# Performance work log

Hardware: AMD Instinct MI355X
Metric: run time of the kernel (lower is better)

The kernel has to match this reference:

```python
import jax, jax.numpy as jnp
import numpy as np

B, C, H, W = 8, 64, 256, 256   # input images
FH, FW = 64, 64                # low-res feature map
S = 256                        # superpixels per image (num[i] == S)


def setup_inputs() -> dict:
    key = jax.random.key(0)
    k1, k2, k3 = jax.random.split(key, 3)
    inp = jax.random.normal(k1, (B, C, H, W), dtype=jnp.float32)
    feat = jax.random.normal(k2, (B, C, FH, FW), dtype=jnp.float32)
    sp = jax.random.randint(k3, (B, 1, H, W), 0, S).astype(jnp.int64)
    num = jnp.full((B,), S, dtype=jnp.int64)
    return {"input": inp, "feature": feat, "sp": sp, "num": num}


def bilinear_align_corners(x, out_h, out_w):
    # F.interpolate(x, size, mode='bilinear', align_corners=True)
    _, _, in_h, in_w = x.shape
    ys = jnp.linspace(0.0, in_h - 1.0, out_h)
    xs = jnp.linspace(0.0, in_w - 1.0, out_w)
    y0 = jnp.floor(ys).astype(jnp.int32)
    x0 = jnp.floor(xs).astype(jnp.int32)
    y1 = jnp.minimum(y0 + 1, in_h - 1)
    x1 = jnp.minimum(x0 + 1, in_w - 1)
    wy = (ys - y0.astype(ys.dtype)).reshape(1, 1, out_h, 1)
    wx = (xs - x0.astype(xs.dtype)).reshape(1, 1, 1, out_w)
    rows = x[:, :, y0, :] * (1.0 - wy) + x[:, :, y1, :] * wy   # [B,C,out_h,in_w]
    return rows[:, :, :, x0] * (1.0 - wx) + rows[:, :, :, x1] * wx


def segment_scalar_means(x, sp, num):
    # torch: mean_values[i][j] = mean(x[i][sp[i]==j]) over channels AND pixels
    b = x.shape[0]
    px = x.mean(axis=1).reshape(b, -1)           # channel-mean per pixel [B, HW]
    ids = sp.reshape(b, -1)                      # [B, HW]
    seg_sum = jax.vmap(lambda v, i: jax.ops.segment_sum(v, i, num_segments=S))(px, ids)
    seg_cnt = jax.vmap(lambda i: jax.ops.segment_sum(jnp.ones(i.shape, jnp.float32), i, num_segments=S))(ids)
    m = jnp.where(seg_cnt > 0, seg_sum / jnp.maximum(seg_cnt, 1.0), 0.0)  # nan_to_num(0)
    valid = jnp.arange(S)[None, :] < num[:, None]                          # j < num[i]
    return jnp.where(valid, m, 0.0)              # [B, S]


def similarity_matrix(m):
    # mean_values broadcast to [B,S,C] => 1 - ||diff||/sqrt(C) == 1 - |m_j - m_k|
    return 1.0 - jnp.abs(m[:, :, None] - m[:, None, :])   # [B, S, S]


def reference(input, feature, sp, num):
    feat = bilinear_align_corners(feature, input.shape[-1], input.shape[-1])
    mat1 = similarity_matrix(segment_scalar_means(input, sp, num))
    mat2 = similarity_matrix(segment_scalar_means(feat, sp, num))
    return jnp.mean(jnp.abs(mat1 - mat2))   # nn.L1Loss()
```

## Files before the change

### kernel.cpp

```cpp
#include <hip/hip_runtime.h>

#define NB 8
#define NC 64
#define NH 256
#define NW 256
#define HW (NH*NW)
#define NFH 64
#define NFW 64
#define FHW (NFH*NFW)
#define NS 256
#define PPB 1024
#define NPB (HW/PPB)
#define NG 4
#define CPG (NC/NG)
#define NA (NB*NPB*NG)
#define NBB (NB*NPB)

__global__ __launch_bounds__(256) void fmean_k(const float* __restrict__ feature,
                                               float* __restrict__ fmean) {
  int idx = blockIdx.x * 256 + threadIdx.x;
  int b = idx >> 10;
  int q = idx & 1023;
  const float4* src = reinterpret_cast<const float4*>(feature + (size_t)b * NC * FHW) + q;
  float4 a = make_float4(0.f, 0.f, 0.f, 0.f);
  #pragma unroll 16
  for (int c = 0; c < NC; ++c) {
    float4 v = src[(size_t)c * (FHW / 4)];
    a.x += v.x; a.y += v.y; a.z += v.z; a.w += v.w;
  }
  const float s = 1.0f / NC;
  a.x *= s; a.y *= s; a.z *= s; a.w *= s;
  reinterpret_cast<float4*>(fmean)[idx] = a;
}

__global__ __launch_bounds__(256) void
main_k(const float* __restrict__ input,
       const int* __restrict__ sp,
       const float* __restrict__ fmean,
       float* __restrict__ part1,
       float* __restrict__ part2,
       float* __restrict__ partc) {
  __shared__ float s_f[FHW];
  __shared__ float s_bins[NS];
  __shared__ unsigned s_cnt[NS];

  const int bid = blockIdx.x;
  const int tid = threadIdx.x;

  if (bid < NA) {
    const int g  = bid & (NG - 1);
    const int pb = (bid >> 2) & (NPB - 1);
    const int b  = bid >> 8;

    s_bins[tid] = 0.f;
    __syncthreads();

    const int p0 = pb * PPB + tid * 4;
    const float* ib = input + ((size_t)(b * NC + g * CPG)) * HW + p0;
    float4 acc = make_float4(0.f, 0.f, 0.f, 0.f);
    #pragma unroll
    for (int c = 0; c < CPG; ++c) {
      float4 v = *reinterpret_cast<const float4*>(ib + (size_t)c * HW);
      acc.x += v.x; acc.y += v.y; acc.z += v.z; acc.w += v.w;
    }
    const float s = 1.0f / NC;
    int4 idv = *reinterpret_cast<const int4*>(sp + (size_t)b * HW + p0);
    atomicAdd(&s_bins[idv.x], acc.x * s);
    atomicAdd(&s_bins[idv.y], acc.y * s);
    atomicAdd(&s_bins[idv.z], acc.z * s);
    atomicAdd(&s_bins[idv.w], acc.w * s);
    __syncthreads();

    part1[(size_t)bid * NS + tid] = s_bins[tid];
  } else {
    const int r  = bid - NA;
    const int b  = r >> 6;
    const int pb = r & (NPB - 1);

    const float4* fsrc = reinterpret_cast<const float4*>(fmean + (size_t)b * FHW);
    #pragma unroll
    for (int i = 0; i < 4; ++i)
      reinterpret_cast<float4*>(s_f)[tid + 256 * i] = fsrc[tid + 256 * i];
    s_bins[tid] = 0.f;
    s_cnt[tid] = 0u;
    __syncthreads();

    const int p0 = pb * PPB + tid * 4;
    int4 idv = *reinterpret_cast<const int4*>(sp + (size_t)b * HW + p0);
    int ids[4] = {idv.x, idv.y, idv.z, idv.w};

    const int h = p0 >> 8;
    const float yd = (float)h * (63.0f / 255.0f);
    const int y0 = (int)yd;
    const float wy = yd - (float)y0;
    const int y1 = min(y0 + 1, NFH - 1);
    const float* row0 = s_f + y0 * NFW;
    const float* row1 = s_f + y1 * NFW;

    #pragma unroll
    for (int i = 0; i < 4; ++i) {
      const int w = (p0 & 255) + i;
      const float xd = (float)w * (63.0f / 255.0f);
      const int x0 = (int)xd;
      const float wx = xd - (float)x0;
      const int x1 = min(x0 + 1, NFW - 1);
      float top = row0[x0] * (1.f - wx) + row0[x1] * wx;
      float bot = row1[x0] * (1.f - wx) + row1[x1] * wx;
      float fv = top * (1.f - wy) + bot * wy;
      atomicAdd(&s_bins[ids[i]], fv);
      atomicAdd(&s_cnt[ids[i]], 1u);
    }
    __syncthreads();

    part2[(size_t)r * NS + tid] = s_bins[tid];
    partc[(size_t)r * NS + tid] = (float)s_cnt[tid];
  }
}

__global__ __launch_bounds__(256) void
finalize_k(const float* __restrict__ part1,
           const float* __restrict__ part2,
           const float* __restrict__ partc,
           const int* __restrict__ num,
           float* __restrict__ partial) {
  __shared__ float m1[NS];
  __shared__ float m2[NS];
  __shared__ float red[256];
  const int b = blockIdx.x;
  const int j = threadIdx.x;

  float s1 = 0.f;
  const float* p1 = part1 + (size_t)b * 256 * NS + j;
  #pragma unroll 8
  for (int t = 0; t < 256; ++t) s1 += p1[(size_t)t * NS];

  float s2 = 0.f, c = 0.f;
  const float* p2 = part2 + (size_t)b * 64 * NS + j;
  const float* pc = partc + (size_t)b * 64 * NS + j;
  #pragma unroll 8
  for (int t = 0; t < 64; ++t) { s2 += p2[(size_t)t * NS]; c += pc[(size_t)t * NS]; }

  const int nb = num[b];
  float v1 = 0.f, v2 = 0.f;
  if (j < nb && c > 0.f) {
    float invc = 1.0f / c;
    v1 = s1 * invc;
    v2 = s2 * invc;
  }
  m1[j] = v1; m2[j] = v2;
  __syncthreads();

  float accum = 0.f;
  #pragma unroll 8
  for (int k = 0; k < NS; ++k) {
    accum += fabsf(fabsf(v1 - m1[k]) - fabsf(v2 - m2[k]));
  }
  red[j] = accum;
  __syncthreads();
  for (int s = 128; s > 0; s >>= 1) {
    if (j < s) red[j] += red[j + s];
    __syncthreads();
  }
  if (j == 0) partial[b] = red[0];
}

__global__ void final_k(const float* __restrict__ partial, float* __restrict__ out) {
  if (threadIdx.x == 0 && blockIdx.x == 0) {
    float s = 0.f;
    for (int b = 0; b < NB; ++b) s += partial[b];
    out[0] = s / (float)((long long)NB * NS * NS);
  }
}

extern "C" void kernel_launch(void* const* d_in, const int* in_sizes, int n_in,
                              void* d_out, int out_size, void* d_ws, size_t ws_size,
                              hipStream_t stream) {
  const float* input   = (const float*)d_in[0];
  const float* feature = (const float*)d_in[1];
  const int*   sp      = (const int*)d_in[2];
  const int*   num     = (const int*)d_in[3];
  float* out = (float*)d_out;

  float* ws      = (float*)d_ws;
  float* part1   = ws;
  float* part2   = ws + (size_t)NA * NS;
  float* partc   = part2 + (size_t)NBB * NS;
  float* fmean   = partc + (size_t)NBB * NS;
  float* partial = fmean + NB * FHW;

  fmean_k<<<32, 256, 0, stream>>>(feature, fmean);
  main_k<<<NA + NBB, 256, 0, stream>>>(input, sp, fmean, part1, part2, partc);
  finalize_k<<<NB, 256, 0, stream>>>(part1, part2, partc, num, partial);
  final_k<<<1, 64, 0, stream>>>(partial, out);
}
```

Before: 56.66 us.

## Widen feature-mean kernel, merge feature blocks into main, fold final reduction

The channel-mean kernel for the feature map now runs on 256 blocks, with each block splitting channels across warps and reducing through shared memory, so it is no longer limited to 32 blocks. The separate feature-binning blocks are merged into the g==0 input blocks, which removes 512 extra blocks but makes those blocks heavier. The last finalize block now does the cross-batch sum using an atomic counter, which drops the final_k launch. The counter is reset inside main_k, and correctness depends on that reset being ordered before finalize runs.

Measured after the change: 63.02 us. 1.11x slower.

```diff
diff --git a/kernel.cpp b/kernel.cpp
--- a/kernel.cpp
+++ b/kernel.cpp
@@ -13,24 +13,38 @@
 #define NPB (HW/PPB)
 #define NG 4
 #define CPG (NC/NG)
-#define NA (NB*NPB*NG)
-#define NBB (NB*NPB)
+#define NMAIN (NB*NPB*NG)
+#define NRB (NB*NPB)
 
 __global__ __launch_bounds__(256) void fmean_k(const float* __restrict__ feature,
                                                float* __restrict__ fmean) {
-  int idx = blockIdx.x * 256 + threadIdx.x;
-  int b = idx >> 10;
-  int q = idx & 1023;
-  const float4* src = reinterpret_cast<const float4*>(feature + (size_t)b * NC * FHW) + q;
+  __shared__ float4 s_p[8][32];
+  const int b     = blockIdx.x >> 5;
+  const int chunk = blockIdx.x & 31;
+  const int q  = threadIdx.x & 31;
+  const int cg = threadIdx.x >> 5;
+
+  const float4* src = reinterpret_cast<const float4*>(
+      feature + (size_t)(b * NC + cg * 8) * FHW) + chunk * 32 + q;
   float4 a = make_float4(0.f, 0.f, 0.f, 0.f);
-  #pragma unroll 16
-  for (int c = 0; c < NC; ++c) {
+  #pragma unroll
+  for (int c = 0; c < 8; ++c) {
     float4 v = src[(size_t)c * (FHW / 4)];
     a.x += v.x; a.y += v.y; a.z += v.z; a.w += v.w;
   }
-  const float s = 1.0f / NC;
-  a.x *= s; a.y *= s; a.z *= s; a.w *= s;
-  reinterpret_cast<float4*>(fmean)[idx] = a;
+  s_p[cg][q] = a;
+  __syncthreads();
+  if (threadIdx.x < 32) {
+    float4 r = make_float4(0.f, 0.f, 0.f, 0.f);
+    #pragma unroll
+    for (int g = 0; g < 8; ++g) {
+      float4 v = s_p[g][threadIdx.x];
+      r.x += v.x; r.y += v.y; r.z += v.z; r.w += v.w;
+    }
+    const float s = 1.0f / NC;
+    r.x *= s; r.y *= s; r.z *= s; r.w *= s;
+    reinterpret_cast<float4*>(fmean + (size_t)b * FHW)[chunk * 32 + threadIdx.x] = r;
+  }
 }
 
 __global__ __launch_bounds__(256) void
@@ -39,56 +53,50 @@
        const float* __restrict__ fmean,
        float* __restrict__ part1,
        float* __restrict__ part2,
-       float* __restrict__ partc) {
+       float* __restrict__ partc,
+       unsigned* __restrict__ counter) {
   __shared__ float s_f[FHW];
   __shared__ float s_bins[NS];
+  __shared__ float s_fb[NS];
   __shared__ unsigned s_cnt[NS];
 
   const int bid = blockIdx.x;
   const int tid = threadIdx.x;
-
-  if (bid < NA) {
-    const int g  = bid & (NG - 1);
-    const int pb = (bid >> 2) & (NPB - 1);
-    const int b  = bid >> 8;
-
-    s_bins[tid] = 0.f;
-    __syncthreads();
-
-    const int p0 = pb * PPB + tid * 4;
-    const float* ib = input + ((size_t)(b * NC + g * CPG)) * HW + p0;
-    float4 acc = make_float4(0.f, 0.f, 0.f, 0.f);
-    #pragma unroll
-    for (int c = 0; c < CPG; ++c) {
-      float4 v = *reinterpret_cast<const float4*>(ib + (size_t)c * HW);
-      acc.x += v.x; acc.y += v.y; acc.z += v.z; acc.w += v.w;
-    }
-    const float s = 1.0f / NC;
-    int4 idv = *reinterpret_cast<const int4*>(sp + (size_t)b * HW + p0);
-    atomicAdd(&s_bins[idv.x], acc.x * s);
-    atomicAdd(&s_bins[idv.y], acc.y * s);
-    atomicAdd(&s_bins[idv.z], acc.z * s);
-    atomicAdd(&s_bins[idv.w], acc.w * s);
-    __syncthreads();
-
-    part1[(size_t)bid * NS + tid] = s_bins[tid];
-  } else {
-    const int r  = bid - NA;
-    const int b  = r >> 6;
-    const int pb = r & (NPB - 1);
-
+  if (bid == 0 && tid == 0) *counter = 0u;
+
+  const int g  = bid & (NG - 1);
+  const int pb = (bid >> 2) & (NPB - 1);
+  const int b  = bid >> 8;
+  const bool roleB = (g == 0);
+
+  s_bins[tid] = 0.f;
+  if (roleB) {
     const float4* fsrc = reinterpret_cast<const float4*>(fmean + (size_t)b * FHW);
     #pragma unroll
     for (int i = 0; i < 4; ++i)
       reinterpret_cast<float4*>(s_f)[tid + 256 * i] = fsrc[tid + 256 * i];
-    s_bins[tid] = 0.f;
+    s_fb[tid] = 0.f;
     s_cnt[tid] = 0u;
-    __syncthreads();
-
-    const int p0 = pb * PPB + tid * 4;
-    int4 idv = *reinterpret_cast<const int4*>(sp + (size_t)b * HW + p0);
-    int ids[4] = {idv.x, idv.y, idv.z, idv.w};
-
+  }
+  __syncthreads();
+
+  const int p0 = pb * PPB + tid * 4;
+  const float* ib = input + (size_t)(b * NC + g * CPG) * HW + p0;
+  float4 acc = make_float4(0.f, 0.f, 0.f, 0.f);
+  #pragma unroll 8
+  for (int c = 0; c < CPG; ++c) {
+    float4 v = *reinterpret_cast<const float4*>(ib + (size_t)c * HW);
+    acc.x += v.x; acc.y += v.y; acc.z += v.z; acc.w += v.w;
+  }
+  const int4 idv = *reinterpret_cast<const int4*>(sp + (size_t)b * HW + p0);
+  const float s = 1.0f / NC;
+  atomicAdd(&s_bins[idv.x], acc.x * s);
+  atomicAdd(&s_bins[idv.y], acc.y * s);
+  atomicAdd(&s_bins[idv.z], acc.z * s);
+  atomicAdd(&s_bins[idv.w], acc.w * s);
+
+  if (roleB) {
+    const int ids[4] = {idv.x, idv.y, idv.z, idv.w};
     const int h = p0 >> 8;
     const float yd = (float)h * (63.0f / 255.0f);
     const int y0 = (int)yd;
@@ -96,7 +104,6 @@
     const int y1 = min(y0 + 1, NFH - 1);
     const float* row0 = s_f + y0 * NFW;
     const float* row1 = s_f + y1 * NFW;
-
     #pragma unroll
     for (int i = 0; i < 4; ++i) {
       const int w = (p0 & 255) + i;
@@ -104,15 +111,19 @@
       const int x0 = (int)xd;
       const float wx = xd - (float)x0;
       const int x1 = min(x0 + 1, NFW - 1);
-      float top = row0[x0] * (1.f - wx) + row0[x1] * wx;
-      float bot = row1[x0] * (1.f - wx) + row1[x1] * wx;
-      float fv = top * (1.f - wy) + bot * wy;
-      atomicAdd(&s_bins[ids[i]], fv);
+      float v0 = row0[x0] * (1.f - wy) + row1[x0] * wy;
+      float v1 = row0[x1] * (1.f - wy) + row1[x1] * wy;
+      float fv = v0 * (1.f - wx) + v1 * wx;
+      atomicAdd(&s_fb[ids[i]], fv);
       atomicAdd(&s_cnt[ids[i]], 1u);
     }
-    __syncthreads();
-
-    part2[(size_t)r * NS + tid] = s_bins[tid];
+  }
+  __syncthreads();
+
+  part1[(size_t)bid * NS + tid] = s_bins[tid];
+  if (roleB) {
+    const int r = (b << 6) | pb;
+    part2[(size_t)r * NS + tid] = s_fb[tid];
     partc[(size_t)r * NS + tid] = (float)s_cnt[tid];
   }
 }
@@ -122,7 +133,9 @@
            const float* __restrict__ part2,
            const float* __restrict__ partc,
            const int* __restrict__ num,
-           float* __restrict__ partial) {
+           float* __restrict__ partial,
+           unsigned* __restrict__ counter,
+           float* __restrict__ out) {
   __shared__ float m1[NS];
   __shared__ float m2[NS];
   __shared__ float red[256];
@@ -157,18 +170,23 @@
   }
   red[j] = accum;
   __syncthreads();
-  for (int s = 128; s > 0; s >>= 1) {
-    if (j < s) red[j] += red[j + s];
+  for (int st = 128; st > 0; st >>= 1) {
+    if (j < st) red[j] += red[j + st];
     __syncthreads();
   }
-  if (j == 0) partial[b] = red[0];
-}
-
-__global__ void final_k(const float* __restrict__ partial, float* __restrict__ out) {
-  if (threadIdx.x == 0 && blockIdx.x == 0) {
-    float s = 0.f;
-    for (int b = 0; b < NB; ++b) s += partial[b];
-    out[0] = s / (float)((long long)NB * NS * NS);
+
+  if (j == 0) {
+    atomicExch(&partial[b], red[0]);
+    __threadfence();
+    unsigned old = atomicAdd(counter, 1u);
+    if (old == NB - 1) {
+      __threadfence();
+      float sAll = 0.f;
+      #pragma unroll
+      for (int i = 0; i < NB; ++i) sAll += atomicAdd(&partial[i], 0.0f);
+      out[0] = sAll / (float)(NB * NS * NS);
+      *counter = 0u;
+    }
   }
 }
 
@@ -182,14 +200,14 @@
   float* out = (float*)d_out;
 
   float* ws      = (float*)d_ws;
-  float* part1   = ws;
-  float* part2   = ws + (size_t)NA * NS;
-  float* partc   = part2 + (size_t)NBB * NS;
-  float* fmean   = partc + (size_t)NBB * NS;
-  float* partial = fmean + NB * FHW;
-
-  fmean_k<<<32, 256, 0, stream>>>(feature, fmean);
-  main_k<<<NA + NBB, 256, 0, stream>>>(input, sp, fmean, part1, part2, partc);
-  finalize_k<<<NB, 256, 0, stream>>>(part1, part2, partc, num, partial);
-  final_k<<<1, 64, 0, stream>>>(partial, out);
-}
+  float*    part1   = ws;
+  float*    part2   = part1 + (size_t)NMAIN * NS;
+  float*    partc   = part2 + (size_t)NRB * NS;
+  float*    fmean   = partc + (size_t)NRB * NS;
+  float*    partial = fmean + NB * FHW;
+  unsigned* counter = (unsigned*)(partial + 8);
+
+  fmean_k<<<NB * 32, 256, 0, stream>>>(feature, fmean);
+  main_k<<<NMAIN, 256, 0, stream>>>(input, sp, fmean, part1, part2, partc, counter);
+  finalize_k<<<NB, 256, 0, stream>>>(part1, part2, partc, num, partial, counter, out);
+}
```
